# Kernel optimization log

Hardware: AMD Instinct MI355X
Metric: run time of the kernel (lower is better)

Reference implementation:

```python
import jax, jax.numpy as jnp
import numpy as np

DIM = 1024
HEADS = 16
NUM_EXPERTS = 8
TOP_K = 2
INNER = 4 * DIM
EPS = 1e-5
NEG = -1e9


def setup_inputs() -> dict:
    key = jax.random.key(0)
    ks = jax.random.split(key, 12)
    s = 0.02
    return {
        "x": jax.random.normal(ks[0], (4, 1024, DIM), dtype=jnp.float32),
        "qkv_w": jax.random.normal(ks[1], (DIM, 3 * DIM), dtype=jnp.float32) * s,
        "out_w": jax.random.normal(ks[2], (DIM, DIM), dtype=jnp.float32) * s,
        "out_b": jnp.zeros((DIM,), dtype=jnp.float32),
        "thresh": jnp.float32(-2.0),
        "ln1_g": jnp.ones((DIM,), dtype=jnp.float32),
        "ln1_b": jnp.zeros((DIM,), dtype=jnp.float32),
        "ln2_g": jnp.ones((DIM,), dtype=jnp.float32),
        "ln2_b": jnp.zeros((DIM,), dtype=jnp.float32),
        "gate_w": jax.random.normal(ks[3], (DIM, NUM_EXPERTS), dtype=jnp.float32) * s,
        "w1": jax.random.normal(ks[4], (NUM_EXPERTS, DIM, INNER), dtype=jnp.float32) * s,
        "b1": jnp.zeros((NUM_EXPERTS, INNER), dtype=jnp.float32),
        "w2": jax.random.normal(ks[5], (NUM_EXPERTS, INNER, DIM), dtype=jnp.float32) * s,
        "b2": jnp.zeros((NUM_EXPERTS, DIM), dtype=jnp.float32),
    }


def _layernorm(x, g, b):
    mu = jnp.mean(x, axis=-1, keepdims=True)
    var = jnp.mean(jnp.square(x - mu), axis=-1, keepdims=True)
    return (x - mu) * jax.lax.rsqrt(var + EPS) * g + b


def reference(x, qkv_w, out_w, out_b, thresh, ln1_g, ln1_b, ln2_g, ln2_b,
              gate_w, w1, b1, w2, b2):
    B, N, D = x.shape
    H = HEADS
    Dh = D // H
    scale = Dh ** -0.5

    # --- Sparse attention (pre-norm, eval mode: dropout off) ---
    h = _layernorm(x, ln1_g, ln1_b)
    qkv = h @ qkv_w                                   # [B,N,3D]
    q, k, v = jnp.split(qkv, 3, axis=-1)
    def heads(t):
        return t.reshape(B, N, H, Dh).transpose(0, 2, 1, 3)  # [B,H,N,Dh]
    q, k, v = heads(q), heads(k), heads(v)
    dots = jnp.einsum("bhid,bhjd->bhij", q, k) * scale
    dots = jnp.where(dots < thresh, jnp.float32(NEG), dots)  # learnable sparsity
    attn = jax.nn.softmax(dots, axis=-1)
    o = jnp.einsum("bhij,bhjd->bhid", attn, v)
    o = o.transpose(0, 2, 1, 3).reshape(B, N, D)
    x = x + o @ out_w + out_b

    # --- MoE FFN (pre-norm) ---
    h2 = _layernorm(x, ln2_g, ln2_b).reshape(-1, D)   # [T,D]
    T = h2.shape[0]
    logits = h2 @ gate_w                              # [T,E]
    probs = jax.nn.softmax(logits, axis=-1)
    aux_loss = NUM_EXPERTS * jnp.sum(probs.mean(0) * probs.sum(0))

    top_w, top_i = jax.lax.top_k(logits, TOP_K)       # [T,k]
    top_w = jax.nn.softmax(top_w, axis=-1)
    # dense combine weights: [T,E], zero for unselected experts
    combine = jnp.zeros((T, NUM_EXPERTS), dtype=h2.dtype)
    combine = combine.at[jnp.arange(T)[:, None], top_i].set(top_w)

    out = jnp.zeros_like(h2)
    for e in range(NUM_EXPERTS):
        y = jax.nn.gelu(h2 @ w1[e] + b1[e], approximate=False) @ w2[e] + b2[e]
        out = out + combine[:, e:e + 1] * y

    x = x + out.reshape(B, N, D)
    return x, aux_loss
```

## Files before the change

kernel.cpp:

```cpp
#include <hip/hip_runtime.h>
#include <math.h>

#define DIM 1024
#define THREE_DIM 3072
#define INNER 4096
#define NTOK 4096
#define NPAIR 8192
#define NEXP 8
#define MAXMB 72

typedef __attribute__((ext_vector_type(8))) short bf16x8;
typedef __attribute__((ext_vector_type(4))) float f32x4;

__device__ __forceinline__ unsigned short f2bf(float f){
    unsigned int x = __float_as_uint(f);
    unsigned int r = x + 0x7fffu + ((x >> 16) & 1u);
    return (unsigned short)(r >> 16);
}

__device__ __forceinline__ unsigned short us4c(ushort4 v, int i){
    return i == 0 ? v.x : (i == 1 ? v.y : (i == 2 ? v.z : v.w));
}

__device__ __forceinline__ void glds16(const void* g, void* l){
    __builtin_amdgcn_global_load_lds(
        (const __attribute__((address_space(1))) void*)g,
        (__attribute__((address_space(3))) void*)l, 16, 0, 0);
}

__device__ __forceinline__ int xcd_swz(){
    int cpx = gridDim.x >> 3;
    return (blockIdx.x & 7) * cpx + (blockIdx.x >> 3);
}

template<int WRITE_BF>
__global__ __launch_bounds__(256)
void ln_kernel(const float* __restrict__ X, const float* __restrict__ g,
               const float* __restrict__ b, float* __restrict__ outF,
               unsigned short* __restrict__ outB)
{
    int row = blockIdx.x;
    int t = threadIdx.x;
    const float4 v = *((const float4*)(X + (size_t)row*DIM) + t);
    float s = v.x + v.y + v.z + v.w;
    #pragma unroll
    for (int m = 1; m < 64; m <<= 1) s += __shfl_xor(s, m, 64);
    __shared__ float red[8];
    int wid = t >> 6, lane = t & 63;
    if (lane == 0) red[wid] = s;
    __syncthreads();
    float mu = (red[0]+red[1]+red[2]+red[3]) * (1.0f/DIM);
    float dx = v.x-mu, dy = v.y-mu, dz = v.z-mu, dw = v.w-mu;
    float s2 = dx*dx + dy*dy + dz*dz + dw*dw;
    #pragma unroll
    for (int m = 1; m < 64; m <<= 1) s2 += __shfl_xor(s2, m, 64);
    if (lane == 0) red[4+wid] = s2;
    __syncthreads();
    float var = (red[4]+red[5]+red[6]+red[7]) * (1.0f/DIM);
    float inv = rsqrtf(var + 1e-5f);
    const float4 gg = *((const float4*)g + t);
    const float4 bb = *((const float4*)b + t);
    float y0 = dx*inv*gg.x + bb.x;
    float y1 = dy*inv*gg.y + bb.y;
    float y2 = dz*inv*gg.z + bb.z;
    float y3 = dw*inv*gg.w + bb.w;
    if (outF){
        float4 o; o.x=y0; o.y=y1; o.z=y2; o.w=y3;
        *((float4*)(outF + (size_t)row*DIM) + t) = o;
    }
    if (WRITE_BF){
        ushort4 u; u.x=f2bf(y0); u.y=f2bf(y1); u.z=f2bf(y2); u.w=f2bf(y3);
        *((ushort4*)(outB + (size_t)row*DIM) + t) = u;
    }
}

template<int MODE>
__global__ __launch_bounds__(256)
void gemm_bf(const unsigned short* __restrict__ A,
             const unsigned short* __restrict__ BT,
             int K, int N, int gnx,
             const float* __restrict__ bias, const float* __restrict__ resid,
             unsigned short* __restrict__ outB, float* __restrict__ outF)
{
    __shared__ __align__(16) unsigned short As[128*64];
    __shared__ __align__(16) unsigned short Bs[128*64];
    int fid = xcd_swz();
    int nx = fid % gnx, my = fid / gnx;
    int m0 = my * 128, n0 = nx * 128;
    int t = threadIdx.x, lane = t & 63, wid = t >> 6;
    size_t aoff[4], boff[4];
    #pragma unroll
    for (int it = 0; it < 4; ++it){
        int chunk = it*256 + wid*64 + lane;
        int r = chunk >> 3, c16 = chunk & 7;
        int c16s = c16 ^ (r & 7);
        aoff[it] = (size_t)(m0 + r)*K + (size_t)(c16s*8);
        boff[it] = (size_t)(n0 + r)*K + (size_t)(c16s*8);
    }
    int wm = wid >> 1, wn = wid & 1;
    f32x4 acc[4][4];
    #pragma unroll
    for (int mi = 0; mi < 4; ++mi)
        #pragma unroll
        for (int ni = 0; ni < 4; ++ni)
            #pragma unroll
            for (int q = 0; q < 4; ++q) acc[mi][ni][q] = 0.f;

    for (int k0 = 0; k0 < K; k0 += 64){
        __syncthreads();
        #pragma unroll
        for (int it = 0; it < 4; ++it){
            glds16(A  + aoff[it] + k0, As + (size_t)(it*256 + wid*64)*8);
            glds16(BT + boff[it] + k0, Bs + (size_t)(it*256 + wid*64)*8);
        }
        __syncthreads();
        bf16x8 af[4][2], bg[4][2];
        #pragma unroll
        for (int mi = 0; mi < 4; ++mi){
            int row = wm*64 + mi*16 + (lane & 15);
            #pragma unroll
            for (int ks = 0; ks < 2; ++ks){
                int cg = (ks*4 + (lane >> 4)) ^ (row & 7);
                af[mi][ks] = *(const bf16x8*)&As[row*64 + cg*8];
            }
        }
        #pragma unroll
        for (int ni = 0; ni < 4; ++ni){
            int row = wn*64 + ni*16 + (lane & 15);
            #pragma unroll
            for (int ks = 0; ks < 2; ++ks){
                int cg = (ks*4 + (lane >> 4)) ^ (row & 7);
                bg[ni][ks] = *(const bf16x8*)&Bs[row*64 + cg*8];
            }
        }
        #pragma unroll
        for (int ks = 0; ks < 2; ++ks)
            #pragma unroll
            for (int mi = 0; mi < 4; ++mi)
                #pragma unroll
                for (int ni = 0; ni < 4; ++ni)
                    acc[mi][ni] = __builtin_amdgcn_mfma_f32_16x16x32_bf16(
                                      af[mi][ks], bg[ni][ks], acc[mi][ni], 0, 0, 0);
    }
    #pragma unroll
    for (int mi = 0; mi < 4; ++mi){
        #pragma unroll
        for (int ni = 0; ni < 4; ++ni){
            int ccol = n0 + wn*64 + ni*16 + (lane & 15);
            #pragma unroll
            for (int j = 0; j < 4; ++j){
                int row = m0 + wm*64 + mi*16 + (lane >> 4)*4 + j;
                float v = acc[mi][ni][j];
                if (MODE == 0){
                    outB[(size_t)row*N + ccol] = f2bf(v);
                } else {
                    outF[(size_t)row*N + ccol] =
                        v + bias[ccol] + resid[(size_t)row*N + ccol];
                }
            }
        }
    }
}

__global__ __launch_bounds__(256)
void attn4_kernel(const unsigned short* __restrict__ qkv,
                  unsigned short* __restrict__ O,
                  const float* __restrict__ threshp)
{
    __shared__ __align__(16) unsigned short Qs[64*64];
    __shared__ __align__(16) unsigned short Ks[64*64];
    __shared__ __align__(16) unsigned short Vp[8*520];
    __shared__ __align__(16) unsigned short Ps[4*1024];

    int fid = xcd_swz();
    int qt = fid & 15, hh = (fid >> 4) & 15, bb = fid >> 8;
    int t = threadIdx.x, lane = t & 63, w = t >> 6;
    int arow = lane & 15, agrp = lane >> 4;
    int qrow0 = bb*1024 + qt*64;
    float thresh = threshp[0];

    #pragma unroll
    for (int it = 0; it < 2; ++it){
        int chunk = it*256 + w*64 + lane;
        int r = chunk >> 3, c16 = chunk & 7;
        glds16(qkv + (size_t)(qrow0+r)*3072 + hh*64 + ((c16 ^ (r & 7))*8),
               Qs + (size_t)(it*256 + w*64)*8);
    }
    __syncthreads();
    bf16x8 qf[2];
    {
        int row = w*16 + arow;
        #pragma unroll
        for (int s = 0; s < 2; ++s){
            int c = (s*4 + agrp) ^ (row & 7);
            qf[s] = *(const bf16x8*)&Qs[row*64 + c*8];
        }
    }

    float m_[4], l_[4];
    f32x4 acc[4];
    #pragma unroll
    for (int j = 0; j < 4; ++j){ m_[j] = -INFINITY; l_[j] = 0.f; }
    #pragma unroll
    for (int d4 = 0; d4 < 4; ++d4)
        #pragma unroll
        for (int j = 0; j < 4; ++j) acc[d4][j] = 0.f;

    for (int kt = 0; kt < 16; ++kt){
        __syncthreads();
        int krow0 = bb*1024 + kt*64;
        #pragma unroll
        for (int it = 0; it < 2; ++it){
            int chunk = it*256 + w*64 + lane;
            int r = chunk >> 3, c16 = chunk & 7;
            glds16(qkv + (size_t)(krow0+r)*3072 + 1024 + hh*64 + ((c16 ^ (r & 7))*8),
                   Ks + (size_t)(it*256 + w*64)*8);
        }
        if (t < 128){
            int jc = t & 7, d0 = (t >> 3) * 4;
            ushort4 u[8];
            #pragma unroll
            for (int jj = 0; jj < 8; ++jj)
                u[jj] = *(const ushort4*)(qkv + (size_t)(krow0 + jc*8 + jj)*3072
                                          + 2048 + hh*64 + d0);
            #pragma unroll
            for (int i = 0; i < 4; ++i){
                ushort4 a, b;
                a.x = us4c(u[0], i); a.y = us4c(u[1], i);
                a.z = us4c(u[2], i); a.w = us4c(u[3], i);
                b.x = us4c(u[4], i); b.y = us4c(u[5], i);
                b.z = us4c(u[6], i); b.w = us4c(u[7], i);
                *(ushort4*)&Vp[jc*520 + (d0+i)*8]     = a;
                *(ushort4*)&Vp[jc*520 + (d0+i)*8 + 4] = b;
            }
        }
        __syncthreads();

        f32x4 sv[4];
        #pragma unroll
        for (int n = 0; n < 4; ++n)
            #pragma unroll
            for (int j = 0; j < 4; ++j) sv[n][j] = 0.f;
        #pragma unroll
        for (int n = 0; n < 4; ++n){
            int krow = n*16 + arow;
            #pragma unroll
            for (int s = 0; s < 2; ++s){
                int c = (s*4 + agrp) ^ (krow & 7);
                bf16x8 kf = *(const bf16x8*)&Ks[krow*64 + c*8];
                sv[n] = __builtin_amdgcn_mfma_f32_16x16x32_bf16(qf[s], kf, sv[n], 0, 0, 0);
            }
        }
        #pragma unroll
        for (int n = 0; n < 4; ++n)
            #pragma unroll
            for (int j = 0; j < 4; ++j){
                float s = sv[n][j] * 0.125f;
                sv[n][j] = (s < thresh) ? -1e9f : s;
            }
        float tmax[4], fac[4], rsum[4];
        #pragma unroll
        for (int j = 0; j < 4; ++j)
            tmax[j] = fmaxf(fmaxf(sv[0][j], sv[1][j]), fmaxf(sv[2][j], sv[3][j]));
        #pragma unroll
        for (int msk = 1; msk < 16; msk <<= 1)
            #pragma unroll
            for (int j = 0; j < 4; ++j)
                tmax[j] = fmaxf(tmax[j], __shfl_xor(tmax[j], msk, 64));
        #pragma unroll
        for (int j = 0; j < 4; ++j){
            float mn = fmaxf(m_[j], tmax[j]);
            fac[j] = __expf(m_[j] - mn);
            m_[j] = mn;
        }
        #pragma unroll
        for (int n = 0; n < 4; ++n)
            #pragma unroll
            for (int j = 0; j < 4; ++j)
                sv[n][j] = __expf(sv[n][j] - m_[j]);
        #pragma unroll
        for (int j = 0; j < 4; ++j)
            rsum[j] = sv[0][j] + sv[1][j] + sv[2][j] + sv[3][j];
        #pragma unroll
        for (int msk = 1; msk < 16; msk <<= 1)
            #pragma unroll
            for (int j = 0; j < 4; ++j)
                rsum[j] += __shfl_xor(rsum[j], msk, 64);
        #pragma unroll
        for (int j = 0; j < 4; ++j)
            l_[j] = l_[j]*fac[j] + rsum[j];
        #pragma unroll
        for (int n = 0; n < 4; ++n){
            int col = n*16 + arow;
            #pragma unroll
            for (int j = 0; j < 4; ++j){
                int r = agrp*4 + j;
                int idx = r*64 + (((col>>3) ^ (r&7)) << 3) + (col & 7);
                Ps[w*1024 + idx] = f2bf(sv[n][j]);
            }
        }
        #pragma unroll
        for (int d4 = 0; d4 < 4; ++d4)
            #pragma unroll
            for (int j = 0; j < 4; ++j) acc[d4][j] *= fac[j];
        #pragma unroll
        for (int s = 0; s < 2; ++s){
            int c = (s*4 + agrp) ^ (arow & 7);
            bf16x8 pa = *(const bf16x8*)&Ps[w*1024 + arow*64 + c*8];
            int jc = s*4 + agrp;
            #pragma unroll
            for (int d4 = 0; d4 < 4; ++d4){
                int dcol = d4*16 + arow;
                bf16x8 vb = *(const bf16x8*)&Vp[jc*520 + dcol*8];
                acc[d4] = __builtin_amdgcn_mfma_f32_16x16x32_bf16(pa, vb, acc[d4], 0, 0, 0);
            }
        }
    }
    #pragma unroll
    for (int j = 0; j < 4; ++j){
        float inv = 1.0f / l_[j];
        int row = qrow0 + w*16 + agrp*4 + j;
        #pragma unroll
        for (int d4 = 0; d4 < 4; ++d4)
            O[(size_t)row*1024 + hh*64 + d4*16 + arow] = f2bf(acc[d4][j] * inv);
    }
}

__global__ __launch_bounds__(64)
void gate_kernel(const float* __restrict__ h2, const float* __restrict__ gw,
                 float* __restrict__ probs, int* __restrict__ top_i,
                 float* __restrict__ top_w)
{
    int tk = blockIdx.x;
    int lane = threadIdx.x;
    const float* hr = h2 + (size_t)tk*DIM;
    float acc[8];
    #pragma unroll
    for (int e = 0; e < 8; ++e) acc[e] = 0.f;
    for (int d = lane; d < DIM; d += 64){
        float hv = hr[d];
        const float* grow = gw + d*8;
        #pragma unroll
        for (int e = 0; e < 8; ++e) acc[e] = fmaf(hv, grow[e], acc[e]);
    }
    #pragma unroll
    for (int m = 1; m < 64; m <<= 1)
        #pragma unroll
        for (int e = 0; e < 8; ++e) acc[e] += __shfl_xor(acc[e], m, 64);
    if (lane == 0){
        float mx = acc[0];
        #pragma unroll
        for (int e = 1; e < 8; ++e) mx = fmaxf(mx, acc[e]);
        float p[8], s = 0.f;
        #pragma unroll
        for (int e = 0; e < 8; ++e){ p[e] = __expf(acc[e]-mx); s += p[e]; }
        float invs = 1.f/s;
        #pragma unroll
        for (int e = 0; e < 8; ++e) probs[(size_t)tk*8+e] = p[e]*invs;
        int i0 = 0; float v0 = acc[0];
        #pragma unroll
        for (int e = 1; e < 8; ++e) if (acc[e] > v0){ v0 = acc[e]; i0 = e; }
        int i1 = -1; float v1 = -INFINITY;
        #pragma unroll
        for (int e = 0; e < 8; ++e) if (e != i0 && acc[e] > v1){ v1 = acc[e]; i1 = e; }
        float w0 = 1.f/(1.f + __expf(v1 - v0));
        top_i[tk*2]   = i0; top_i[tk*2+1] = i1;
        top_w[tk*2]   = w0; top_w[tk*2+1] = 1.f - w0;
    }
}

__global__ __launch_bounds__(256)
void aux_kernel(const float* __restrict__ probs, float* __restrict__ dout)
{
    int t = threadIdx.x;
    float acc[8];
    #pragma unroll
    for (int e = 0; e < 8; ++e) acc[e] = 0.f;
    for (int r = t; r < NTOK; r += 256){
        const float* pr = probs + (size_t)r*8;
        #pragma unroll
        for (int e = 0; e < 8; ++e) acc[e] += pr[e];
    }
    #pragma unroll
    for (int m = 1; m < 64; m <<= 1)
        #pragma unroll
        for (int e = 0; e < 8; ++e) acc[e] += __shfl_xor(acc[e], m, 64);
    __shared__ float red[4][8];
    int wid = t >> 6, lane = t & 63;
    if (lane == 0)
        for (int e = 0; e < 8; ++e) red[wid][e] = acc[e];
    __syncthreads();
    if (t == 0){
        float aux = 0.f;
        for (int e = 0; e < 8; ++e){
            float S = red[0][e]+red[1][e]+red[2][e]+red[3][e];
            aux += S*S;
        }
        dout[(size_t)NTOK*DIM] = aux * (8.0f/NTOK);
    }
}

__global__ __launch_bounds__(512)
void routing_kernel(const int* __restrict__ topi, int* __restrict__ perm,
                    int* __restrict__ mblk_e)
{
    __shared__ int cnt[8];
    __shared__ int obase[8];
    int t = threadIdx.x, w = t >> 6, lane = t & 63;
    int c = 0;
    for (int i0 = 0; i0 < NPAIR; i0 += 64){
        int e = topi[i0 + lane];
        c += (e == w) ? 1 : 0;
    }
    #pragma unroll
    for (int m = 1; m < 64; m <<= 1) c += __shfl_xor(c, m, 64);
    if (lane == 0) cnt[w] = c;
    __syncthreads();
    if (t == 0){
        int mb = 0;
        for (int e = 0; e < 8; ++e){
            obase[e] = mb*128;
            int nb = (cnt[e] + 127) >> 7;
            for (int k = 0; k < nb; ++k) mblk_e[mb++] = e;
        }
        for (; mb < MAXMB; ++mb) mblk_e[mb] = -1;
    }
    __syncthreads();
    for (int i = t; i < MAXMB*128; i += 512) perm[i] = -1;
    __syncthreads();
    int base = obase[w];
    for (int i0 = 0; i0 < NPAIR; i0 += 64){
        int p = i0 + lane;
        int e = topi[p];
        bool mt = (e == w);
        unsigned long long mk = __ballot(mt);
        int rank = __popcll(mk & ((1ull << lane) - 1ull));
        if (mt) perm[base + rank] = p;
        base += __popcll(mk);
    }
}

template<int MODE>
__global__ __launch_bounds__(256)
void gemm_moe2(const unsigned short* __restrict__ Abase,
               const unsigned short* __restrict__ BTbase,
               int K, int N, int lda,
               const int* __restrict__ perm, const int* __restrict__ mblk_e,
               const float* __restrict__ bias,
               unsigned short* __restrict__ actout,
               const float* __restrict__ topw, float* __restrict__ dout)
{
    const int GNX = (MODE == 2) ? (INNER/128) : (DIM/128);
    const int KSP = (MODE == 2) ? 1 : 2;
    int fid = xcd_swz();
    int nx = fid % GNX;
    int rest = fid / GNX;
    int mb = rest % MAXMB;
    int kk = rest / MAXMB;
    int e = mblk_e[mb];
    if (e < 0) return;
    int kspan = K / KSP, kbeg = kk * kspan, kend = kbeg + kspan;

    __shared__ __align__(16) unsigned short As[128*64];
    __shared__ __align__(16) unsigned short Bs[128*64];
    __shared__ int permL[128];
    int t = threadIdx.x;
    if (t < 128) permL[t] = perm[mb*128 + t];
    __syncthreads();
    int lane = t & 63, wid = t >> 6;
    int n0 = nx * 128;
    const unsigned short* BT = BTbase + (size_t)e * (size_t)N * (size_t)K;
    int base_chunk = wid*64 + lane;
    size_t aoff[4], boff[4];
    #pragma unroll
    for (int it = 0; it < 4; ++it){
        int chunk = base_chunk + it*256;
        int r = chunk >> 3, c16 = chunk & 7;
        int c16s = c16 ^ (r & 7);
        size_t ar;
        if (MODE == 2){ int p = permL[r]; ar = (p >= 0) ? (size_t)(p >> 1) : 0; }
        else          { ar = (size_t)(mb*128 + r); }
        aoff[it] = ar*(size_t)lda + (size_t)(c16s*8);
        boff[it] = (size_t)(n0 + r)*(size_t)K + (size_t)(c16s*8);
    }
    int wm = wid >> 1, wn = wid & 1;
    f32x4 acc[4][4];
    #pragma unroll
    for (int mi = 0; mi < 4; ++mi)
        #pragma unroll
        for (int ni = 0; ni < 4; ++ni)
            #pragma unroll
            for (int q = 0; q < 4; ++q) acc[mi][ni][q] = 0.f;

    for (int k0 = kbeg; k0 < kend; k0 += 64){
        __syncthreads();
        #pragma unroll
        for (int it = 0; it < 4; ++it){
            glds16(Abase + aoff[it] + k0, As + (size_t)(wid*64 + it*256)*8);
            glds16(BT    + boff[it] + k0, Bs + (size_t)(wid*64 + it*256)*8);
        }
        __syncthreads();
        bf16x8 af[4][2], bg[4][2];
        #pragma unroll
        for (int mi = 0; mi < 4; ++mi){
            int row = wm*64 + mi*16 + (lane & 15);
            #pragma unroll
            for (int ks = 0; ks < 2; ++ks){
                int cg = (ks*4 + (lane >> 4)) ^ (row & 7);
                af[mi][ks] = *(const bf16x8*)&As[row*64 + cg*8];
            }
        }
        #pragma unroll
        for (int ni = 0; ni < 4; ++ni){
            int row = wn*64 + ni*16 + (lane & 15);
            #pragma unroll
            for (int ks = 0; ks < 2; ++ks){
                int cg = (ks*4 + (lane >> 4)) ^ (row & 7);
                bg[ni][ks] = *(const bf16x8*)&Bs[row*64 + cg*8];
            }
        }
        #pragma unroll
        for (int ks = 0; ks < 2; ++ks)
            #pragma unroll
            for (int mi = 0; mi < 4; ++mi)
                #pragma unroll
                for (int ni = 0; ni < 4; ++ni)
                    acc[mi][ni] = __builtin_amdgcn_mfma_f32_16x16x32_bf16(
                                      af[mi][ks], bg[ni][ks], acc[mi][ni], 0, 0, 0);
    }
    #pragma unroll
    for (int mi = 0; mi < 4; ++mi){
        #pragma unroll
        for (int ni = 0; ni < 4; ++ni){
            int ccol = n0 + wn*64 + ni*16 + (lane & 15);
            float bv = (kk == 0) ? bias[(size_t)e*N + ccol] : 0.f;
            #pragma unroll
            for (int j = 0; j < 4; ++j){
                int rloc = wm*64 + mi*16 + (lane >> 4)*4 + j;
                float v = acc[mi][ni][j];
                if (MODE == 2){
                    float gx = v + bv;
                    float z2 = gx * fmaf(gx*gx, 0.07135481283f, 1.595769122f);
                    float ex = __expf(-z2);
                    float gl = gx * __builtin_amdgcn_rcpf(1.0f + ex);
                    actout[(size_t)(mb*128 + rloc)*N + ccol] = f2bf(gl);
                } else {
                    int p = permL[rloc];
                    if (p >= 0){
                        float val = (v + bv) * topw[p];
                        atomicAdd(&dout[(size_t)(p >> 1)*N + ccol], val);
                    }
                }
            }
        }
    }
}

__global__ __launch_bounds__(256)
void transp_cast(const float* __restrict__ W, unsigned short* __restrict__ WT,
                 int K, int N)
{
    __shared__ float tile[32][33];
    size_t base = (size_t)blockIdx.z * (size_t)K * (size_t)N;
    const float* Wp = W + base;
    unsigned short* Tp = WT + base;
    int t = threadIdx.x;
    int r = t >> 3, c4 = (t & 7) << 2;
    int n0 = blockIdx.x << 5, k0 = blockIdx.y << 5;
    float4 v = *(const float4*)(Wp + (size_t)(k0+r)*N + n0 + c4);
    tile[r][c4+0] = v.x; tile[r][c4+1] = v.y;
    tile[r][c4+2] = v.z; tile[r][c4+3] = v.w;
    __syncthreads();
    ushort4 u;
    u.x = f2bf(tile[c4+0][r]);
    u.y = f2bf(tile[c4+1][r]);
    u.z = f2bf(tile[c4+2][r]);
    u.w = f2bf(tile[c4+3][r]);
    *(ushort4*)(Tp + (size_t)(n0+r)*K + k0 + c4) = u;
}

extern "C" void kernel_launch(void* const* d_in, const int* in_sizes, int n_in,
                              void* d_out, int out_size, void* d_ws, size_t ws_size,
                              hipStream_t stream)
{
    const float* x      = (const float*)d_in[0];
    const float* qkv_w  = (const float*)d_in[1];
    const float* out_w  = (const float*)d_in[2];
    const float* out_b  = (const float*)d_in[3];
    const float* thresh = (const float*)d_in[4];
    const float* ln1_g  = (const float*)d_in[5];
    const float* ln1_b  = (const float*)d_in[6];
    const float* ln2_g  = (const float*)d_in[7];
    const float* ln2_b  = (const float*)d_in[8];
    const float* gate_w = (const float*)d_in[9];
    const float* w1     = (const float*)d_in[10];
    const float* b1     = (const float*)d_in[11];
    const float* w2     = (const float*)d_in[12];
    const float* b2     = (const float*)d_in[13];
    float* out = (float*)d_out;
    char* ws = (char*)d_ws;

    const size_t MB = (size_t)1 << 20;
    unsigned short* h1bf  = (unsigned short*)(ws);
    unsigned short* qkvbf = (unsigned short*)(ws + 8*MB);
    unsigned short* obf   = (unsigned short*)(ws + 32*MB);
    float*          h2    = (float*)(ws + 40*MB);
    unsigned short* h2bf  = (unsigned short*)(ws + 56*MB);
    unsigned short* qwT   = (unsigned short*)(ws + 64*MB);
    unsigned short* owT   = (unsigned short*)(ws + 70*MB);
    unsigned short* w1T   = (unsigned short*)(ws + 72*MB);
    unsigned short* w2T   = (unsigned short*)(ws + 136*MB);
    unsigned short* act   = (unsigned short*)(ws + 200*MB);
    float* probs          = (float*)(ws + 276*MB);
    int*   top_i          = (int*)(ws + 276*MB + 131072);
    float* top_w          = (float*)(ws + 276*MB + 163840);
    int*   perm           = (int*)(ws + 276*MB + 196608);
    int*   mblk           = (int*)(ws + 276*MB + 237568);

    transp_cast<<<dim3(THREE_DIM/32, DIM/32, 1), 256, 0, stream>>>(qkv_w, qwT, DIM, THREE_DIM);
    transp_cast<<<dim3(DIM/32, DIM/32, 1), 256, 0, stream>>>(out_w, owT, DIM, DIM);

    ln_kernel<1><<<NTOK, 256, 0, stream>>>(x, ln1_g, ln1_b, nullptr, h1bf);
    gemm_bf<0><<<(THREE_DIM/128)*(NTOK/128), 256, 0, stream>>>(
        h1bf, qwT, DIM, THREE_DIM, THREE_DIM/128, nullptr, nullptr, qkvbf, nullptr);
    attn4_kernel<<<16*16*4, 256, 0, stream>>>(qkvbf, obf, thresh);
    gemm_bf<1><<<(DIM/128)*(NTOK/128), 256, 0, stream>>>(
        obf, owT, DIM, DIM, DIM/128, out_b, x, nullptr, out);
    ln_kernel<1><<<NTOK, 256, 0, stream>>>(out, ln2_g, ln2_b, h2, h2bf);
    gate_kernel<<<NTOK, 64, 0, stream>>>(h2, gate_w, probs, top_i, top_w);
    aux_kernel<<<1, 256, 0, stream>>>(probs, out);
    routing_kernel<<<1, 512, 0, stream>>>(top_i, perm, mblk);

    transp_cast<<<dim3(INNER/32, DIM/32, NEXP), 256, 0, stream>>>(w1, w1T, DIM, INNER);
    transp_cast<<<dim3(DIM/32, INNER/32, NEXP), 256, 0, stream>>>(w2, w2T, INNER, DIM);

    gemm_moe2<2><<<(INNER/128)*MAXMB, 256, 0, stream>>>(
        h2bf, w1T, DIM, INNER, DIM, perm, mblk, b1, act, nullptr, nullptr);
    gemm_moe2<3><<<(DIM/128)*MAXMB*2, 256, 0, stream>>>(
        act, w2T, INNER, DIM, INNER, perm, mblk, b2, nullptr, top_w, out);
}
```

Before: 553.1 us.

## Replace MoE down-proj atomic scatter with partial buffers and combine kernel

The second expert GEMM no longer scatters weighted results into the output with float atomicAdd. Instead each K-split half writes its un-weighted result to a dense partial buffer indexed by expert slot. A new combine kernel then gathers the two slots per token, applies the top-k weights and adds them into the output. This is meant to avoid contended global atomics and makes the sum deterministic, at the cost of roughly 75 MB of extra partial-buffer writes and reads plus one more kernel launch, and it needs a larger workspace.

```diff
diff --git a/kernel.cpp b/kernel.cpp
--- a/kernel.cpp
+++ b/kernel.cpp
@@ -8,6 +8,7 @@
 #define NPAIR 8192
 #define NEXP 8
 #define MAXMB 72
+#define PARTROWS (MAXMB*128)
 
 typedef __attribute__((ext_vector_type(8))) short bf16x8;
 typedef __attribute__((ext_vector_type(4))) float f32x4;
@@ -402,7 +403,7 @@
 
 __global__ __launch_bounds__(512)
 void routing_kernel(const int* __restrict__ topi, int* __restrict__ perm,
-                    int* __restrict__ mblk_e)
+                    int* __restrict__ mblk_e, int* __restrict__ tokslot)
 {
     __shared__ int cnt[8];
     __shared__ int obase[8];
@@ -435,7 +436,10 @@
         bool mt = (e == w);
         unsigned long long mk = __ballot(mt);
         int rank = __popcll(mk & ((1ull << lane) - 1ull));
-        if (mt) perm[base + rank] = p;
+        if (mt){
+            perm[base + rank] = p;
+            tokslot[p] = base + rank;
+        }
         base += __popcll(mk);
     }
 }
@@ -448,10 +452,9 @@
                const int* __restrict__ perm, const int* __restrict__ mblk_e,
                const float* __restrict__ bias,
                unsigned short* __restrict__ actout,
-               const float* __restrict__ topw, float* __restrict__ dout)
+               float* __restrict__ partout)
 {
     const int GNX = (MODE == 2) ? (INNER/128) : (DIM/128);
-    const int KSP = (MODE == 2) ? 1 : 2;
     int fid = xcd_swz();
     int nx = fid % GNX;
     int rest = fid / GNX;
@@ -459,13 +462,14 @@
     int kk = rest / MAXMB;
     int e = mblk_e[mb];
     if (e < 0) return;
-    int kspan = K / KSP, kbeg = kk * kspan, kend = kbeg + kspan;
+    int kspan = (MODE == 2) ? K : (K >> 1);
+    int kbeg = kk * kspan, kend = kbeg + kspan;
 
     __shared__ __align__(16) unsigned short As[128*64];
     __shared__ __align__(16) unsigned short Bs[128*64];
     __shared__ int permL[128];
     int t = threadIdx.x;
-    if (t < 128) permL[t] = perm[mb*128 + t];
+    if (MODE == 2 && t < 128) permL[t] = perm[mb*128 + t];
     __syncthreads();
     int lane = t & 63, wid = t >> 6;
     int n0 = nx * 128;
@@ -545,15 +549,34 @@
                     float gl = gx * __builtin_amdgcn_rcpf(1.0f + ex);
                     actout[(size_t)(mb*128 + rloc)*N + ccol] = f2bf(gl);
                 } else {
-                    int p = permL[rloc];
-                    if (p >= 0){
-                        float val = (v + bv) * topw[p];
-                        atomicAdd(&dout[(size_t)(p >> 1)*N + ccol], val);
-                    }
+                    partout[((size_t)kk*PARTROWS + mb*128 + rloc)*N + ccol] = v + bv;
                 }
             }
         }
     }
+}
+
+__global__ __launch_bounds__(256)
+void combine_kernel(const float* __restrict__ part,
+                    const int* __restrict__ tokslot,
+                    const float* __restrict__ topw,
+                    float* __restrict__ out)
+{
+    int tk = blockIdx.x, t = threadIdx.x;
+    int s0 = tokslot[tk*2], s1 = tokslot[tk*2+1];
+    float w0 = topw[tk*2], w1 = topw[tk*2+1];
+    const float4* p00 = (const float4*)(part + (size_t)s0*DIM) + t;
+    const float4* p10 = (const float4*)(part + ((size_t)PARTROWS + s0)*DIM) + t;
+    const float4* p01 = (const float4*)(part + (size_t)s1*DIM) + t;
+    const float4* p11 = (const float4*)(part + ((size_t)PARTROWS + s1)*DIM) + t;
+    float4* o4 = (float4*)(out + (size_t)tk*DIM) + t;
+    float4 a0 = *p00, a1 = *p10, b0 = *p01, b1 = *p11;
+    float4 o = *o4;
+    o.x += w0*(a0.x + a1.x) + w1*(b0.x + b1.x);
+    o.y += w0*(a0.y + a1.y) + w1*(b0.y + b1.y);
+    o.z += w0*(a0.z + a1.z) + w1*(b0.z + b1.z);
+    o.w += w0*(a0.w + a1.w) + w1*(b0.w + b1.w);
+    *o4 = o;
 }
 
 __global__ __launch_bounds__(256)
@@ -616,6 +639,8 @@
     float* top_w          = (float*)(ws + 276*MB + 163840);
     int*   perm           = (int*)(ws + 276*MB + 196608);
     int*   mblk           = (int*)(ws + 276*MB + 237568);
+    int*   tokslot        = (int*)(ws + 276*MB + 241664);
+    float* part           = (float*)(ws + 280*MB);
 
     transp_cast<<<dim3(THREE_DIM/32, DIM/32, 1), 256, 0, stream>>>(qkv_w, qwT, DIM, THREE_DIM);
     transp_cast<<<dim3(DIM/32, DIM/32, 1), 256, 0, stream>>>(out_w, owT, DIM, DIM);
@@ -629,13 +654,14 @@
     ln_kernel<1><<<NTOK, 256, 0, stream>>>(out, ln2_g, ln2_b, h2, h2bf);
     gate_kernel<<<NTOK, 64, 0, stream>>>(h2, gate_w, probs, top_i, top_w);
     aux_kernel<<<1, 256, 0, stream>>>(probs, out);
-    routing_kernel<<<1, 512, 0, stream>>>(top_i, perm, mblk);
+    routing_kernel<<<1, 512, 0, stream>>>(top_i, perm, mblk, tokslot);
 
     transp_cast<<<dim3(INNER/32, DIM/32, NEXP), 256, 0, stream>>>(w1, w1T, DIM, INNER);
     transp_cast<<<dim3(DIM/32, INNER/32, NEXP), 256, 0, stream>>>(w2, w2T, INNER, DIM);
 
     gemm_moe2<2><<<(INNER/128)*MAXMB, 256, 0, stream>>>(
-        h2bf, w1T, DIM, INNER, DIM, perm, mblk, b1, act, nullptr, nullptr);
+        h2bf, w1T, DIM, INNER, DIM, perm, mblk, b1, act, nullptr);
     gemm_moe2<3><<<(DIM/128)*MAXMB*2, 256, 0, stream>>>(
-        act, w2T, INNER, DIM, INNER, perm, mblk, b2, nullptr, top_w, out);
-}
+        act, w2T, INNER, DIM, INNER, perm, mblk, b2, nullptr, part);
+    combine_kernel<<<NTOK, 256, 0, stream>>>(part, tokslot, top_w, out);
+}
```

New measurement: 524.1 us. 5.2% less time.
